# Kernel tuning notes

Measured on AMD Instinct MI355X. Metric: run time of the kernel, lower is better.

## Reference

```python
import jax, jax.numpy as jnp
import numpy as np

CODEBOOK_SIZE = 8192
CODEBOOK_DIM = 1024
HIDDEN_DIM = 4096
OUT_DIM = 1024
B, M = 32, 576


def setup_inputs() -> dict:
    key = jax.random.key(0)
    k_idx, k_cb, k_w1, k_w2 = jax.random.split(key, 4)
    index = jax.random.randint(k_idx, (B, M), 0, CODEBOOK_SIZE, dtype=jnp.int32)
    # codebook initialized as sqrt(d) * randn, as in the torch module
    codebook = (CODEBOOK_DIM ** 0.5) * jax.random.normal(k_cb, (CODEBOOK_SIZE, CODEBOOK_DIM), dtype=jnp.float32)
    s1 = 1.0 / np.sqrt(CODEBOOK_DIM)
    s2 = 1.0 / np.sqrt(HIDDEN_DIM)
    W1 = s1 * jax.random.normal(k_w1, (CODEBOOK_DIM, HIDDEN_DIM), dtype=jnp.float32)
    b1 = jnp.zeros((HIDDEN_DIM,), dtype=jnp.float32)
    W2 = s2 * jax.random.normal(k_w2, (HIDDEN_DIM, OUT_DIM), dtype=jnp.float32)
    b2 = jnp.zeros((OUT_DIM,), dtype=jnp.float32)
    return {"index": index, "codebook": codebook, "W1": W1, "b1": b1, "W2": W2, "b2": b2}


def reference(index, codebook, W1, b1, W2, b2):
    # one_hot(index) @ codebook is mathematically an index gather:
    # quantized[b, m, :] = codebook[index[b, m], :]
    quantized = jnp.take(codebook, index, axis=0)  # [B, M, D]
    # Decoder_ff: 2-layer GELU MLP (D -> 4D -> D)
    h = jax.nn.gelu(jnp.einsum('bmd,dh->bmh', quantized, W1) + b1)
    rec = jnp.einsum('bmh,ho->bmo', h, W2) + b2
    return rec
```

## Files before the change

### kernel.cpp

```cpp
#include <hip/hip_runtime.h>
#include <stdint.h>

typedef __attribute__((ext_vector_type(8))) short s16x8;
typedef __attribute__((ext_vector_type(4))) float f32x4;

__device__ __forceinline__ short f2bf(float x) {
  uint32_t u = __builtin_bit_cast(uint32_t, x);
  u += 0x7FFFu + ((u >> 16) & 1u);
  return (short)(u >> 16);
}

__device__ __forceinline__ void gload16(void* l, const void* g) {
  __builtin_amdgcn_global_load_lds(
      (const __attribute__((address_space(1))) void*)g,
      (__attribute__((address_space(3))) void*)l, 16, 0, 0);
}

__device__ __forceinline__ float gelu_tanh(float x) {
  float u = 0.7978845608028654f * (x + 0.044715f * x * x * x);
  float e = __expf(2.0f * u);
  return x - x / (e + 1.0f);
}

__global__ void gather_cvt(const float* __restrict__ cb, const int* __restrict__ idx,
                           short* __restrict__ out) {
  int m = blockIdx.x * 2 + (threadIdx.x >> 7);
  int c = (threadIdx.x & 127) * 8;
  const float* s = cb + (size_t)idx[m] * 1024 + c;
  s16x8 o;
#pragma unroll
  for (int j = 0; j < 8; ++j) o[j] = f2bf(s[j]);
  *(s16x8*)(out + (size_t)m * 1024 + c) = o;
}

__global__ void cvt_T(const float* __restrict__ in, short* __restrict__ out, int K, int N) {
  int Kb = K >> 3;
  int t = blockIdx.x * 256 + threadIdx.x;
  if (t >= N * Kb) return;
  int n = t / Kb;
  int k8 = (t - n * Kb) * 8;
  const float* s = in + (size_t)k8 * N + n;
  s16x8 o;
#pragma unroll
  for (int j = 0; j < 8; ++j) o[j] = f2bf(s[(size_t)j * N]);
  *(s16x8*)(out + (size_t)n * K + k8) = o;
}

template <int MODE, int K, int N, int BN>
__global__ __launch_bounds__(512, 2) void gemm8p(
    const short* __restrict__ A, const short* __restrict__ Bt,
    const float* __restrict__ bias, void* __restrict__ Cv) {
  constexpr int NIH = BN / 128;
  constexpr int RB = BN / 64;
  constexpr int ATS = 16384;
  constexpr int LDSH = (256 + BN) * 64;
  __shared__ short lds[2 * LDSH];

  constexpr int NBN = N / BN;
  const int nwg = gridDim.x;
  int swz = blockIdx.x;
  swz = (swz & 7) * (nwg >> 3) + (swz >> 3);
  const int bm = swz / NBN, bn = swz - (swz / NBN) * NBN;

  const int tid = threadIdx.x;
  const int wid = tid >> 6, lane = tid & 63;
  const int wr = wid >> 2, wc = wid & 3;
  const int lr = lane & 15, hi = lane >> 4;

  const int sl = (tid & 7) ^ ((tid >> 3) & 7);
  const short* aptr[4];
  const short* bptr[RB];
#pragma unroll
  for (int r = 0; r < 4; ++r)
    aptr[r] = A + (long)(bm * 256 + r * 64 + (tid >> 3)) * K + sl * 8;
#pragma unroll
  for (int r = 0; r < RB; ++r)
    bptr[r] = Bt + (long)(bn * BN + r * 64 + (tid >> 3)) * K + sl * 8;
  const int wlds = wid * 512;

  const int aRB = (wr * 128 + lr) * 64;
  const int bRB = ATS + (wc * (BN / 4) + lr) * 64;
  const int sk0 = ((0 + hi) ^ (lr & 7)) * 8;
  const int sk1 = ((4 + hi) ^ (lr & 7)) * 8;

  f32x4 acc[8][2 * NIH] = {};
  s16x8 af[4][2], bf[2][NIH][2];

  constexpr int NT = K >> 6;

#pragma unroll
  for (int r = 0; r < RB; ++r) gload16(&lds[ATS + r * 4096 + wlds], bptr[r]);
  gload16(&lds[0 * 4096 + wlds], aptr[0]);
  gload16(&lds[2 * 4096 + wlds], aptr[2]);
  gload16(&lds[1 * 4096 + wlds], aptr[1]);
  gload16(&lds[3 * 4096 + wlds], aptr[3]);
  asm volatile("s_waitcnt vmcnt(2)" ::: "memory");
  __builtin_amdgcn_s_barrier();

  for (int t = 0; t < NT; ++t) {
    const int cb = (t & 1) * LDSH;
    const int nb = LDSH - cb;
    const int kt = ((t + 1 < NT) ? (t + 1) : 0) << 6;

#pragma unroll
    for (int mi = 0; mi < 4; ++mi) {
      af[mi][0] = *(const s16x8*)&lds[cb + aRB + mi * 1024 + sk0];
      af[mi][1] = *(const s16x8*)&lds[cb + aRB + mi * 1024 + sk1];
    }
#pragma unroll
    for (int ni = 0; ni < NIH; ++ni) {
      bf[0][ni][0] = *(const s16x8*)&lds[cb + bRB + ni * 1024 + sk0];
      bf[0][ni][1] = *(const s16x8*)&lds[cb + bRB + ni * 1024 + sk1];
    }
#pragma unroll
    for (int r = 0; r < RB / 2; ++r)
      gload16(&lds[nb + ATS + r * 4096 + wlds], bptr[r] + kt);
    __builtin_amdgcn_s_barrier();
    asm volatile("s_waitcnt lgkmcnt(0)" ::: "memory");
    __builtin_amdgcn_s_setprio(1);
#pragma unroll
    for (int mi = 0; mi < 4; ++mi)
#pragma unroll
      for (int ni = 0; ni < NIH; ++ni)
#pragma unroll
        for (int ks = 0; ks < 2; ++ks)
          acc[mi][ni] = __builtin_amdgcn_mfma_f32_16x16x32_bf16(af[mi][ks], bf[0][ni][ks], acc[mi][ni], 0, 0, 0);
    __builtin_amdgcn_s_setprio(0);
    __builtin_amdgcn_s_barrier();

#pragma unroll
    for (int ni = 0; ni < NIH; ++ni) {
      bf[1][ni][0] = *(const s16x8*)&lds[cb + bRB + (NIH + ni) * 1024 + sk0];
      bf[1][ni][1] = *(const s16x8*)&lds[cb + bRB + (NIH + ni) * 1024 + sk1];
    }
#pragma unroll
    for (int r = RB / 2; r < RB; ++r)
      gload16(&lds[nb + ATS + r * 4096 + wlds], bptr[r] + kt);
    __builtin_amdgcn_s_barrier();
    asm volatile("s_waitcnt lgkmcnt(0)" ::: "memory");
    __builtin_amdgcn_s_setprio(1);
#pragma unroll
    for (int mi = 0; mi < 4; ++mi)
#pragma unroll
      for (int ni = 0; ni < NIH; ++ni)
#pragma unroll
        for (int ks = 0; ks < 2; ++ks)
          acc[mi][NIH + ni] = __builtin_amdgcn_mfma_f32_16x16x32_bf16(af[mi][ks], bf[1][ni][ks], acc[mi][NIH + ni], 0, 0, 0);
    __builtin_amdgcn_s_setprio(0);
    if constexpr (RB == 4) asm volatile("s_waitcnt vmcnt(4)" ::: "memory");
    else                   asm volatile("s_waitcnt vmcnt(2)" ::: "memory");
    __builtin_amdgcn_s_barrier();

#pragma unroll
    for (int mi = 0; mi < 4; ++mi) {
      af[mi][0] = *(const s16x8*)&lds[cb + aRB + 4096 + mi * 1024 + sk0];
      af[mi][1] = *(const s16x8*)&lds[cb + aRB + 4096 + mi * 1024 + sk1];
    }
    gload16(&lds[nb + 0 * 4096 + wlds], aptr[0] + kt);
    gload16(&lds[nb + 2 * 4096 + wlds], aptr[2] + kt);
    __builtin_amdgcn_s_barrier();
    asm volatile("s_waitcnt lgkmcnt(0)" ::: "memory");
    __builtin_amdgcn_s_setprio(1);
#pragma unroll
    for (int mi = 0; mi < 4; ++mi)
#pragma unroll
      for (int ni = 0; ni < NIH; ++ni)
#pragma unroll
        for (int ks = 0; ks < 2; ++ks)
          acc[4 + mi][ni] = __builtin_amdgcn_mfma_f32_16x16x32_bf16(af[mi][ks], bf[0][ni][ks], acc[4 + mi][ni], 0, 0, 0);
    __builtin_amdgcn_s_setprio(0);
    __builtin_amdgcn_s_barrier();

    gload16(&lds[nb + 1 * 4096 + wlds], aptr[1] + kt);
    gload16(&lds[nb + 3 * 4096 + wlds], aptr[3] + kt);
    __builtin_amdgcn_s_barrier();
    __builtin_amdgcn_s_setprio(1);
#pragma unroll
    for (int mi = 0; mi < 4; ++mi)
#pragma unroll
      for (int ni = 0; ni < NIH; ++ni)
#pragma unroll
        for (int ks = 0; ks < 2; ++ks)
          acc[4 + mi][NIH + ni] = __builtin_amdgcn_mfma_f32_16x16x32_bf16(af[mi][ks], bf[1][ni][ks], acc[4 + mi][NIH + ni], 0, 0, 0);
    __builtin_amdgcn_s_setprio(0);
    asm volatile("s_waitcnt vmcnt(2)" ::: "memory");
    __builtin_amdgcn_s_barrier();
  }

  const int m0 = bm * 256 + wr * 128 + hi * 4;
  const int n0 = bn * BN + wc * (BN / 4) + lr;
#pragma unroll
  for (int j = 0; j < 2 * NIH; ++j) {
    const int n = n0 + j * 16;
    const float bv = bias[n];
#pragma unroll
    for (int i = 0; i < 8; ++i) {
      f32x4 v = acc[i][j];
#pragma unroll
      for (int r = 0; r < 4; ++r) {
        const int m = m0 + i * 16 + r;
        float x = v[r] + bv;
        if (MODE == 1) {
          ((short*)Cv)[(size_t)m * N + n] = f2bf(gelu_tanh(x));
        } else {
          ((float*)Cv)[(size_t)m * N + n] = x;
        }
      }
    }
  }
}

extern "C" void kernel_launch(void* const* d_in, const int* in_sizes, int n_in,
                              void* d_out, int out_size, void* d_ws, size_t ws_size,
                              hipStream_t stream) {
  const int* idx = (const int*)d_in[0];
  const float* cb = (const float*)d_in[1];
  const float* W1 = (const float*)d_in[2];
  const float* b1 = (const float*)d_in[3];
  const float* W2 = (const float*)d_in[4];
  const float* b2 = (const float*)d_in[5];
  float* out = (float*)d_out;

  const int Mtot = 32 * 576;

  char* ws = (char*)d_ws;
  short* aq = (short*)(ws);
  short* w1t = (short*)(ws + (size_t)40 * 1024 * 1024);
  short* w2t = (short*)(ws + (size_t)48 * 1024 * 1024);
  short* h = (short*)(ws + (size_t)56 * 1024 * 1024);

  gather_cvt<<<Mtot / 2, 256, 0, stream>>>(cb, idx, aq);
  cvt_T<<<2048, 256, 0, stream>>>(W1, w1t, 1024, 4096);
  cvt_T<<<2048, 256, 0, stream>>>(W2, w2t, 4096, 1024);

  size_t avail = (ws_size > (size_t)56 * 1024 * 1024) ? ws_size - (size_t)56 * 1024 * 1024 : 0;
  int nc = 1;
  while (nc < 8 && (size_t)(Mtot / nc) * 8192 > avail) nc <<= 1;
  const int Mc = Mtot / nc;

  for (int c = 0; c < nc; ++c) {
    gemm8p<1, 1024, 4096, 256><<<(Mc / 256) * 16, 512, 0, stream>>>(
        aq + (size_t)c * Mc * 1024, w1t, b1, (void*)h);
    gemm8p<2, 4096, 1024, 128><<<(Mc / 256) * 8, 512, 0, stream>>>(
        h, w2t, b2, (void*)(out + (size_t)c * Mc * 1024));
  }
}
```

Measured before the change: 492.8 us.

## Use 288x256 GEMM tiles so workgroup count matches CU count

Both GEMMs now use a single 288x256 tile shape, replacing the old 256-row tiles with 256 or 128 columns. With Mtot=18432 this gives 64*16=1024 and 64*4=256 workgroups, which is intended to remove the partial-wave tail that 72*16=1152 and 72*8=576 tiles left on 256 CUs. The second GEMM also gets a wider N tile, improving reuse. The extra 32 rows are loaded by half the waves into a new LDS region; the other waves load into a dummy scratch area. This raises register use (9x4 accumulators) and LDS size, which may hurt occupancy under launch_bounds(512,2).

```diff
diff --git a/kernel.cpp b/kernel.cpp
--- a/kernel.cpp
+++ b/kernel.cpp
@@ -46,15 +46,14 @@
   *(s16x8*)(out + (size_t)n * K + k8) = o;
 }
 
-template <int MODE, int K, int N, int BN>
+template <int MODE, int K, int N>
 __global__ __launch_bounds__(512, 2) void gemm8p(
     const short* __restrict__ A, const short* __restrict__ Bt,
     const float* __restrict__ bias, void* __restrict__ Cv) {
-  constexpr int NIH = BN / 128;
-  constexpr int RB = BN / 64;
-  constexpr int ATS = 16384;
-  constexpr int LDSH = (256 + BN) * 64;
-  __shared__ short lds[2 * LDSH];
+  constexpr int BM = 288, BN = 256;
+  constexpr int ATS = BM * 64;
+  constexpr int LDSH = (BM + BN) * 64;
+  __shared__ short lds[2 * LDSH + 2048];
 
   constexpr int NBN = N / BN;
   const int nwg = gridDim.x;
@@ -68,32 +67,30 @@
   const int lr = lane & 15, hi = lane >> 4;
 
   const int sl = (tid & 7) ^ ((tid >> 3) & 7);
-  const short* aptr[4];
-  const short* bptr[RB];
-#pragma unroll
-  for (int r = 0; r < 4; ++r)
-    aptr[r] = A + (long)(bm * 256 + r * 64 + (tid >> 3)) * K + sl * 8;
-#pragma unroll
-  for (int r = 0; r < RB; ++r)
-    bptr[r] = Bt + (long)(bn * BN + r * 64 + (tid >> 3)) * K + sl * 8;
+  const long rstep = (long)64 * K;
+  const short* aptr0 = A + (long)(bm * BM + (tid >> 3)) * K + sl * 8;
+  const short* aptr4 = A + (long)(bm * BM + 256 + ((tid >> 3) & 31)) * K + sl * 8;
+  const short* bptr0 = Bt + (long)(bn * BN + (tid >> 3)) * K + sl * 8;
   const int wlds = wid * 512;
-
-  const int aRB = (wr * 128 + lr) * 64;
-  const int bRB = ATS + (wc * (BN / 4) + lr) * 64;
+  const int a4rel = (wid < 4) ? (16384 + wid * 512) : -1;
+
+  const int aRB = (wr * 144 + lr) * 64;
+  const int bRB = ATS + (wc * 64 + lr) * 64;
   const int sk0 = ((0 + hi) ^ (lr & 7)) * 8;
   const int sk1 = ((4 + hi) ^ (lr & 7)) * 8;
 
-  f32x4 acc[8][2 * NIH] = {};
-  s16x8 af[4][2], bf[2][NIH][2];
+  f32x4 acc[9][4] = {};
+  s16x8 af[5][2], bf[2][2][2];
 
   constexpr int NT = K >> 6;
 
 #pragma unroll
-  for (int r = 0; r < RB; ++r) gload16(&lds[ATS + r * 4096 + wlds], bptr[r]);
-  gload16(&lds[0 * 4096 + wlds], aptr[0]);
-  gload16(&lds[2 * 4096 + wlds], aptr[2]);
-  gload16(&lds[1 * 4096 + wlds], aptr[1]);
-  gload16(&lds[3 * 4096 + wlds], aptr[3]);
+  for (int r = 0; r < 4; ++r) gload16(&lds[ATS + r * 4096 + wlds], bptr0 + r * rstep);
+  gload16(&lds[0 * 4096 + wlds], aptr0 + 0 * rstep);
+  gload16(&lds[2 * 4096 + wlds], aptr0 + 2 * rstep);
+  gload16(&lds[3 * 4096 + wlds], aptr0 + 3 * rstep);
+  gload16(&lds[1 * 4096 + wlds], aptr0 + 1 * rstep);
+  gload16((a4rel >= 0) ? &lds[a4rel] : &lds[2 * LDSH + (wid & 3) * 512], aptr4);
   asm volatile("s_waitcnt vmcnt(2)" ::: "memory");
   __builtin_amdgcn_s_barrier();
 
@@ -108,20 +105,19 @@
       af[mi][1] = *(const s16x8*)&lds[cb + aRB + mi * 1024 + sk1];
     }
 #pragma unroll
-    for (int ni = 0; ni < NIH; ++ni) {
+    for (int ni = 0; ni < 2; ++ni) {
       bf[0][ni][0] = *(const s16x8*)&lds[cb + bRB + ni * 1024 + sk0];
       bf[0][ni][1] = *(const s16x8*)&lds[cb + bRB + ni * 1024 + sk1];
     }
-#pragma unroll
-    for (int r = 0; r < RB / 2; ++r)
-      gload16(&lds[nb + ATS + r * 4096 + wlds], bptr[r] + kt);
+    gload16(&lds[nb + ATS + 0 * 4096 + wlds], bptr0 + 0 * rstep + kt);
+    gload16(&lds[nb + ATS + 1 * 4096 + wlds], bptr0 + 1 * rstep + kt);
     __builtin_amdgcn_s_barrier();
     asm volatile("s_waitcnt lgkmcnt(0)" ::: "memory");
     __builtin_amdgcn_s_setprio(1);
 #pragma unroll
     for (int mi = 0; mi < 4; ++mi)
 #pragma unroll
-      for (int ni = 0; ni < NIH; ++ni)
+      for (int ni = 0; ni < 2; ++ni)
 #pragma unroll
         for (int ks = 0; ks < 2; ++ks)
           acc[mi][ni] = __builtin_amdgcn_mfma_f32_16x16x32_bf16(af[mi][ks], bf[0][ni][ks], acc[mi][ni], 0, 0, 0);
@@ -129,72 +125,71 @@
     __builtin_amdgcn_s_barrier();
 
 #pragma unroll
-    for (int ni = 0; ni < NIH; ++ni) {
-      bf[1][ni][0] = *(const s16x8*)&lds[cb + bRB + (NIH + ni) * 1024 + sk0];
-      bf[1][ni][1] = *(const s16x8*)&lds[cb + bRB + (NIH + ni) * 1024 + sk1];
-    }
-#pragma unroll
-    for (int r = RB / 2; r < RB; ++r)
-      gload16(&lds[nb + ATS + r * 4096 + wlds], bptr[r] + kt);
+    for (int ni = 0; ni < 2; ++ni) {
+      bf[1][ni][0] = *(const s16x8*)&lds[cb + bRB + (2 + ni) * 1024 + sk0];
+      bf[1][ni][1] = *(const s16x8*)&lds[cb + bRB + (2 + ni) * 1024 + sk1];
+    }
+    gload16(&lds[nb + ATS + 2 * 4096 + wlds], bptr0 + 2 * rstep + kt);
+    gload16(&lds[nb + ATS + 3 * 4096 + wlds], bptr0 + 3 * rstep + kt);
     __builtin_amdgcn_s_barrier();
     asm volatile("s_waitcnt lgkmcnt(0)" ::: "memory");
     __builtin_amdgcn_s_setprio(1);
 #pragma unroll
     for (int mi = 0; mi < 4; ++mi)
 #pragma unroll
-      for (int ni = 0; ni < NIH; ++ni)
-#pragma unroll
-        for (int ks = 0; ks < 2; ++ks)
-          acc[mi][NIH + ni] = __builtin_amdgcn_mfma_f32_16x16x32_bf16(af[mi][ks], bf[1][ni][ks], acc[mi][NIH + ni], 0, 0, 0);
-    __builtin_amdgcn_s_setprio(0);
-    if constexpr (RB == 4) asm volatile("s_waitcnt vmcnt(4)" ::: "memory");
-    else                   asm volatile("s_waitcnt vmcnt(2)" ::: "memory");
-    __builtin_amdgcn_s_barrier();
-
-#pragma unroll
-    for (int mi = 0; mi < 4; ++mi) {
-      af[mi][0] = *(const s16x8*)&lds[cb + aRB + 4096 + mi * 1024 + sk0];
-      af[mi][1] = *(const s16x8*)&lds[cb + aRB + 4096 + mi * 1024 + sk1];
-    }
-    gload16(&lds[nb + 0 * 4096 + wlds], aptr[0] + kt);
-    gload16(&lds[nb + 2 * 4096 + wlds], aptr[2] + kt);
+      for (int ni = 0; ni < 2; ++ni)
+#pragma unroll
+        for (int ks = 0; ks < 2; ++ks)
+          acc[mi][2 + ni] = __builtin_amdgcn_mfma_f32_16x16x32_bf16(af[mi][ks], bf[1][ni][ks], acc[mi][2 + ni], 0, 0, 0);
+    __builtin_amdgcn_s_setprio(0);
+    asm volatile("s_waitcnt vmcnt(4)" ::: "memory");
+    __builtin_amdgcn_s_barrier();
+
+#pragma unroll
+    for (int mi = 0; mi < 5; ++mi) {
+      af[mi][0] = *(const s16x8*)&lds[cb + aRB + (4 + mi) * 1024 + sk0];
+      af[mi][1] = *(const s16x8*)&lds[cb + aRB + (4 + mi) * 1024 + sk1];
+    }
+    gload16(&lds[nb + 0 * 4096 + wlds], aptr0 + 0 * rstep + kt);
+    gload16(&lds[nb + 2 * 4096 + wlds], aptr0 + 2 * rstep + kt);
+    gload16(&lds[nb + 3 * 4096 + wlds], aptr0 + 3 * rstep + kt);
     __builtin_amdgcn_s_barrier();
     asm volatile("s_waitcnt lgkmcnt(0)" ::: "memory");
     __builtin_amdgcn_s_setprio(1);
 #pragma unroll
-    for (int mi = 0; mi < 4; ++mi)
-#pragma unroll
-      for (int ni = 0; ni < NIH; ++ni)
+    for (int mi = 0; mi < 5; ++mi)
+#pragma unroll
+      for (int ni = 0; ni < 2; ++ni)
 #pragma unroll
         for (int ks = 0; ks < 2; ++ks)
           acc[4 + mi][ni] = __builtin_amdgcn_mfma_f32_16x16x32_bf16(af[mi][ks], bf[0][ni][ks], acc[4 + mi][ni], 0, 0, 0);
     __builtin_amdgcn_s_setprio(0);
     __builtin_amdgcn_s_barrier();
 
-    gload16(&lds[nb + 1 * 4096 + wlds], aptr[1] + kt);
-    gload16(&lds[nb + 3 * 4096 + wlds], aptr[3] + kt);
-    __builtin_amdgcn_s_barrier();
-    __builtin_amdgcn_s_setprio(1);
-#pragma unroll
-    for (int mi = 0; mi < 4; ++mi)
-#pragma unroll
-      for (int ni = 0; ni < NIH; ++ni)
-#pragma unroll
-        for (int ks = 0; ks < 2; ++ks)
-          acc[4 + mi][NIH + ni] = __builtin_amdgcn_mfma_f32_16x16x32_bf16(af[mi][ks], bf[1][ni][ks], acc[4 + mi][NIH + ni], 0, 0, 0);
+    gload16(&lds[nb + 1 * 4096 + wlds], aptr0 + 1 * rstep + kt);
+    gload16((a4rel >= 0) ? &lds[nb + a4rel] : &lds[2 * LDSH + (wid & 3) * 512], aptr4 + kt);
+    __builtin_amdgcn_s_barrier();
+    __builtin_amdgcn_s_setprio(1);
+#pragma unroll
+    for (int mi = 0; mi < 5; ++mi)
+#pragma unroll
+      for (int ni = 0; ni < 2; ++ni)
+#pragma unroll
+        for (int ks = 0; ks < 2; ++ks)
+          acc[4 + mi][2 + ni] = __builtin_amdgcn_mfma_f32_16x16x32_bf16(af[mi][ks], bf[1][ni][ks], acc[4 + mi][2 + ni], 0, 0, 0);
     __builtin_amdgcn_s_setprio(0);
     asm volatile("s_waitcnt vmcnt(2)" ::: "memory");
     __builtin_amdgcn_s_barrier();
   }
 
-  const int m0 = bm * 256 + wr * 128 + hi * 4;
-  const int n0 = bn * BN + wc * (BN / 4) + lr;
-#pragma unroll
-  for (int j = 0; j < 2 * NIH; ++j) {
+  const int m0 = bm * BM + wr * 144 + hi * 4;
+  const int n0 = bn * BN + wc * 64 + lr;
+#pragma unroll
+  for (int j = 0; j < 4; ++j) {
     const int n = n0 + j * 16;
     const float bv = bias[n];
 #pragma unroll
-    for (int i = 0; i < 8; ++i) {
+    for (int i = 0; i < 9; ++i) {
       f32x4 v = acc[i][j];
 #pragma unroll
       for (int r = 0; r < 4; ++r) {
@@ -239,9 +234,9 @@
   const int Mc = Mtot / nc;
 
   for (int c = 0; c < nc; ++c) {
-    gemm8p<1, 1024, 4096, 256><<<(Mc / 256) * 16, 512, 0, stream>>>(
+    gemm8p<1, 1024, 4096><<<(Mc / 288) * 16, 512, 0, stream>>>(
         aq + (size_t)c * Mc * 1024, w1t, b1, (void*)h);
-    gemm8p<2, 4096, 1024, 128><<<(Mc / 256) * 8, 512, 0, stream>>>(
+    gemm8p<2, 4096, 1024><<<(Mc / 288) * 4, 512, 0, stream>>>(
         h, w2t, b2, (void*)(out + (size_t)c * Mc * 1024));
   }
 }
```

New measurement: 395.9 us. -19.7%, faster.
